# Kernel optimization log

Hardware: AMD Instinct MI355X
Metric: run time of the kernel (lower is better)

## Reference

```python
import jax, jax.numpy as jnp
import numpy as np

HIST, CNTX, PRED = 336, 168, 24
C = 1            # c_in == c_out == 1 (univariate)
HID = 128        # GRU hidden size
NFEAT = 5        # hourly time features (freq_map['H'])
EMB = 10 * NFEAT # embedding_dim * freq_map['H'] = 50
NLAGS = HIST - CNTX            # 168 lag taps
IN_DIM = EMB + NLAGS           # rnn input size = 218
NSAMP = 8192     # num_parallel_samples


def setup_inputs() -> dict:
    key = jax.random.key(0)
    ks = jax.random.split(key, 8)
    s = lambda fan: 1.0 / np.sqrt(fan)
    return {
        "x": jax.random.normal(ks[0], (1, HIST, C), jnp.float32),
        "x_mark": jax.random.normal(ks[1], (1, HIST, NFEAT), jnp.float32),
        "y_mark": jax.random.normal(ks[2], (1, PRED, NFEAT), jnp.float32),
        "W_emb": jax.random.normal(ks[3], (NFEAT, EMB), jnp.float32) * s(NFEAT),
        "b_emb": jnp.zeros((EMB,), jnp.float32),
        "W_ih": jax.random.normal(ks[4], (3 * HID, IN_DIM), jnp.float32) * s(IN_DIM),
        "W_hh": jax.random.normal(ks[5], (3 * HID, HID), jnp.float32) * s(HID),
        "b_ih": jnp.zeros((3 * HID,), jnp.float32),
        "b_hh": jnp.zeros((3 * HID,), jnp.float32),
        "W_proj": jax.random.normal(ks[6], (HID, 3), jnp.float32) * s(HID),
        "b_proj": jnp.zeros((3,), jnp.float32),
        "mode": 0,
    }


def reference(x, x_mark, y_mark, W_emb, b_emb, W_ih, W_hh, b_ih, b_hh, W_proj, b_proj, mode):

    def gru_step(h, xt):  # PyTorch GRU cell semantics (gate order r,z,n)
        gi = xt @ W_ih.T + b_ih
        gh = h @ W_hh.T + b_hh
        i_r, i_z, i_n = jnp.split(gi, 3, axis=-1)
        h_r, h_z, h_n = jnp.split(gh, 3, axis=-1)
        r = jax.nn.sigmoid(i_r + h_r)
        z = jax.nn.sigmoid(i_z + h_z)
        n = jnp.tanh(i_n + r * h_n)
        return (1.0 - z) * n + z * h

    B = x.shape[0]  # 1
    # ----- unroll_encoder (y=None path) -----
    # mean_abs_scaling over last cntx_len steps
    scale = jnp.clip(jnp.mean(jnp.abs(x[:, -CNTX:, :]), axis=1, keepdims=True), 1e-5, None)  # (B,1,C)
    xs = x / scale  # scaled sequence (lags/scale == lags of scaled sequence)
    # lagged subsequences: lag indices 1..NLAGS, subsequence length CNTX
    t_idx = (HIST - CNTX) + jnp.arange(CNTX)[:, None] - jnp.arange(1, NLAGS + 1)[None, :]  # (CNTX, NLAGS)
    lags = xs[:, t_idx, 0]  # (B, CNTX, NLAGS)  (C==1 so flatten is trivial)
    tf = x_mark[:, HIST - CNTX:, :] @ W_emb + b_emb  # (B, CNTX, EMB)
    enc_in = jnp.concatenate([lags, tf], axis=-1)  # (B, CNTX, IN_DIM)
    h0 = jnp.zeros((B, HID), x.dtype)
    h_last, _ = jax.lax.scan(lambda h, xt: (gru_step(h, xt), None), h0,
                             jnp.swapaxes(enc_in, 0, 1))  # final GRU state (B,HID)

    # ----- sampling_decoder -----
    sc = scale[0, 0, 0]  # scalar (B=1, C=1)
    h = jnp.broadcast_to(h_last, (NSAMP, HID))                       # repeat state over samples
    ym = jnp.broadcast_to(y_mark @ W_emb + b_emb, (NSAMP, PRED, EMB))  # repeated embedded marks
    buf = jnp.broadcast_to(x[0, -NLAGS:, 0], (NSAMP, NLAGS))         # last NLAGS observed values
    key0 = jax.random.key(42)

    def step(carry, ym_k):
        buf, h, key = carry
        key, sk = jax.random.split(key)
        lag_in = buf[:, ::-1] / sc                 # decoder lags: most recent first
        xin = jnp.concatenate([lag_in, ym_k], axis=-1)  # (S, IN_DIM)
        h = gru_step(h, xin)
        p = h @ W_proj + b_proj                    # (S, 3) StudentT arg projection
        df = 2.0 + jax.nn.softplus(p[:, 0])
        loc = p[:, 1]
        sigma = jax.nn.softplus(p[:, 2])
        t = jax.random.t(sk, df, shape=df.shape)
        samp = (loc + sigma * t) * sc              # affine-transformed StudentT sample
        buf = jnp.concatenate([buf[:, 1:], samp[:, None]], axis=1)
        return (buf, h, key), samp

    _, samples = jax.lax.scan(step, (buf, h, key0), jnp.swapaxes(ym, 0, 1))  # (PRED, S)
    return samples.T[:, :, None]  # (num_parallel_samples, pred_len, c_out)
```

## Files before the change

kernel.cpp:

```cpp
#include <hip/hip_runtime.h>
#include <stdint.h>

#define HIST 336
#define CNTX 168
#define PRED 24
#define HID 128
#define NFEAT 5
#define EMB 50
#define NLAGS 168
#define IN_DIM 218
#define NSAMP 8192
#define G3 384

#define WS_XS     0
#define WS_SC     336
#define WS_TF     340
#define WS_YM     8740
#define WS_KEYS   9940
#define WS_ENCGI  10036
#define WS_WQ     10036
#define WS_GISH   74548
#define WS_HLAST  83764
#define WS_WIHT   83892

__device__ __forceinline__ uint32_t rotl32(uint32_t v, int r){ return (v<<r)|(v>>(32-r)); }

__device__ __forceinline__ void threefry(uint32_t k0, uint32_t k1, uint32_t x0, uint32_t x1,
                                         uint32_t &o0, uint32_t &o1){
  uint32_t ks2 = k0 ^ k1 ^ 0x1BD11BDAu;
  x0 += k0; x1 += k1;
#define TFR(a) { x0 += x1; x1 = rotl32(x1,(a)); x1 ^= x0; }
  TFR(13) TFR(15) TFR(26) TFR(6)
  x0 += k1; x1 += ks2 + 1u;
  TFR(17) TFR(29) TFR(16) TFR(24)
  x0 += ks2; x1 += k0 + 2u;
  TFR(13) TFR(15) TFR(26) TFR(6)
  x0 += k0; x1 += k1 + 3u;
  TFR(17) TFR(29) TFR(16) TFR(24)
  x0 += k1; x1 += ks2 + 4u;
  TFR(13) TFR(15) TFR(26) TFR(6)
  x0 += ks2; x1 += k0 + 5u;
#undef TFR
  o0 = x0; o1 = x1;
}

__device__ __forceinline__ void tf_split2(uint32_t k0, uint32_t k1,
                                          uint32_t &a0, uint32_t &a1,
                                          uint32_t &b0, uint32_t &b1){
  threefry(k0,k1, 0u,0u, a0,a1);
  threefry(k0,k1, 0u,1u, b0,b1);
}

__device__ __forceinline__ void tf_split3(uint32_t k0, uint32_t k1,
                                          uint32_t &a0, uint32_t &a1,
                                          uint32_t &b0, uint32_t &b1,
                                          uint32_t &c0, uint32_t &c1){
  threefry(k0,k1, 0u,0u, a0,a1);
  threefry(k0,k1, 0u,1u, b0,b1);
  threefry(k0,k1, 0u,2u, c0,c1);
}

__device__ __forceinline__ uint32_t tf_bits1(uint32_t k0, uint32_t k1){
  uint32_t o0,o1; threefry(k0,k1, 0u,0u, o0,o1); return o0 ^ o1;
}

__device__ __forceinline__ uint32_t tf_bits_at(uint32_t k0, uint32_t k1, uint32_t i){
  uint32_t o0,o1; threefry(k0,k1, 0u,i, o0,o1); return o0 ^ o1;
}

__device__ __forceinline__ float bits_to_f01(uint32_t b){
  return __uint_as_float((b>>9) | 0x3f800000u) - 1.0f;
}

__device__ __forceinline__ float erfinv32(float x){
  float w = -log1pf(-x*x);
  float p;
  if (w < 5.0f){
    w = w - 2.5f;
    p = 2.81022636e-08f;
    p = fmaf(p, w, 3.43273939e-07f);
    p = fmaf(p, w, -3.5233877e-06f);
    p = fmaf(p, w, -4.39150654e-06f);
    p = fmaf(p, w, 0.00021858087f);
    p = fmaf(p, w, -0.00125372503f);
    p = fmaf(p, w, -0.00417768164f);
    p = fmaf(p, w, 0.246640727f);
    p = fmaf(p, w, 1.50140941f);
  } else {
    w = sqrtf(w) - 3.0f;
    p = -0.000200214257f;
    p = fmaf(p, w, 0.000100950558f);
    p = fmaf(p, w, 0.00134934322f);
    p = fmaf(p, w, -0.00367342844f);
    p = fmaf(p, w, 0.00573950773f);
    p = fmaf(p, w, -0.0076224613f);
    p = fmaf(p, w, 0.00943887047f);
    p = fmaf(p, w, 1.00167406f);
    p = fmaf(p, w, 2.83297682f);
  }
  return p*x;
}

__device__ __forceinline__ float normal_from_key(uint32_t k0, uint32_t k1){
  uint32_t b = tf_bits1(k0,k1);
  const float lo = -0.99999994f;
  float f = bits_to_f01(b);
  float u = fmaxf(lo, f*2.0f + lo);
  return 1.41421356f * erfinv32(u);
}

__device__ float gamma_sample(uint32_t k0, uint32_t k1, float alpha){
  float d = __fsub_rn(alpha, 0.33333334f);
  float c = 0.33333334f / sqrtf(d);
  uint32_t ck0,ck1, sb0,sb1;
  tf_split2(k0,k1, ck0,ck1, sb0,sb1);
  float V;
  for(;;){
    uint32_t nk0,nk1, xk0,xk1, uk0,uk1;
    tf_split3(ck0,ck1, nk0,nk1, xk0,xk1, uk0,uk1);
    ck0=nk0; ck1=nk1;
    float x, v;
    do {
      uint32_t xa0,xa1, xb0,xb1;
      tf_split2(xk0,xk1, xa0,xa1, xb0,xb1);
      xk0=xa0; xk1=xa1;
      x = normal_from_key(xb0,xb1);
      v = __fadd_rn(1.0f, __fmul_rn(x, c));
    } while (v <= 0.0f);
    float X  = __fmul_rn(x, x);
    float Vv = __fmul_rn(__fmul_rn(v, v), v);
    float U  = bits_to_f01(tf_bits1(uk0,uk1));
    float t1 = __fsub_rn(1.0f, __fmul_rn(0.0331f, __fmul_rn(X, X)));
    bool cont = (U >= t1);
    if (cont){
      float lhs = logf(U);
      float rhs = __fadd_rn(__fmul_rn(0.5f, X),
                  __fmul_rn(d, __fadd_rn(__fsub_rn(1.0f, Vv), logf(Vv))));
      cont = (lhs >= rhs);
    }
    if (!cont){ V = Vv; break; }
  }
  return d*V;
}

__device__ __forceinline__ float softplus_f(float x){
  float amax = fmaxf(x, 0.0f);
  return amax + log1pf(expf(-fabsf(x)));
}

__global__ __launch_bounds__(256) void k1_prep(const float* __restrict__ x,
                                               const float* __restrict__ xmark,
                                               const float* __restrict__ ymark,
                                               const float* __restrict__ Wemb,
                                               const float* __restrict__ bemb,
                                               float* __restrict__ ws){
  __shared__ float red[256];
  __shared__ float s_sc;
  int t = threadIdx.x;
  float a = 0.f;
  if (t < CNTX) a = fabsf(x[CNTX + t]);
  red[t] = a;
  __syncthreads();
  for(int s=128; s>0; s>>=1){ if(t<s) red[t]+=red[t+s]; __syncthreads(); }
  if (t==0){ s_sc = fmaxf(red[0]/168.0f, 1e-5f); ws[WS_SC]=s_sc; }
  __syncthreads();
  float sc = s_sc;
  for(int i=t; i<HIST; i+=256) ws[WS_XS+i] = x[i]/sc;
  for(int idx=t; idx<CNTX*EMB; idx+=256){
    int tt = idx/EMB, e = idx%EMB;
    float acc = bemb[e];
    for(int f=0; f<NFEAT; f++) acc += xmark[(CNTX+tt)*NFEAT+f]*Wemb[f*EMB+e];
    ws[WS_TF+idx] = acc;
  }
  for(int idx=t; idx<PRED*EMB; idx+=256){
    int kk = idx/EMB, e = idx%EMB;
    float acc = bemb[e];
    for(int f=0; f<NFEAT; f++) acc += ymark[kk*NFEAT+f]*Wemb[f*EMB+e];
    ws[WS_YM+idx] = acc;
  }
  if (t==0){
    uint32_t* kp = reinterpret_cast<uint32_t*>(ws + WS_KEYS);
    uint32_t c0 = 0u, c1 = 42u;
    for(int k=0;k<PRED;k++){
      uint32_t a0,a1,b0,b1;
      tf_split2(c0,c1, a0,a1, b0,b1);
      c0=a0; c1=a1;
      uint32_t n0,n1,g0,g1;
      tf_split2(b0,b1, n0,n1, g0,g1);
      kp[k*4+0]=n0; kp[k*4+1]=n1; kp[k*4+2]=g0; kp[k*4+3]=g1;
    }
  }
}

__global__ __launch_bounds__(256) void k2_gi(const float* __restrict__ Wih,
                                             const float* __restrict__ bih,
                                             const float* __restrict__ bhh,
                                             float* __restrict__ ws){
  int idx = blockIdx.x*256 + threadIdx.x;
  if (idx >= 192*G3) return;
  int t = idx / G3, r = idx % G3;
  const float* wr = Wih + r*IN_DIM;
  const float* xs = ws + WS_XS;
  float acc = bih[r] + (r < 256 ? bhh[r] : 0.0f);
  if (t < CNTX){
    const float* tf = ws + WS_TF + t*EMB;
    for(int j=0;j<NLAGS;j++) acc += wr[j]*xs[CNTX + t - 1 - j];
    for(int e=0;e<EMB;e++)   acc += wr[NLAGS+e]*tf[e];
    ws[WS_ENCGI + t*G3 + r] = acc;
  } else {
    int k = t - CNTX;
    const float* ym = ws + WS_YM + k*EMB;
    for(int e=0;e<EMB;e++)   acc += wr[NLAGS+e]*ym[e];
    for(int i=k;i<NLAGS;i++) acc += wr[i]*xs[HIST-1-i+k];
    ws[WS_GISH + k*G3 + r] = acc;
  }
}

__global__ __launch_bounds__(256) void k2b_wiht(const float* __restrict__ Wih,
                                                float* __restrict__ ws){
  int idx = blockIdx.x*256 + threadIdx.x;
  if (idx >= PRED*G3) return;
  int r = idx / PRED, i = idx % PRED;
  ws[WS_WIHT + i*G3 + r] = Wih[r*IN_DIM + i];
}

__global__ __launch_bounds__(384) void k3_enc(const float* __restrict__ Whh,
                                              const float* __restrict__ bhh,
                                              float* __restrict__ ws){
  __shared__ __align__(16) float h[HID];
  __shared__ float grz[256];
  __shared__ float hnv[HID];
  int r = threadIdx.x;
  float4 w[32];
  const float4* wr = (const float4*)(Whh + r*HID);
  #pragma unroll
  for(int i=0;i<32;i++) w[i] = wr[i];
  float bh = (r>=256)? bhh[r] : 0.0f;
  if (r < HID) h[r] = 0.0f;
  __syncthreads();
  const float* encgi = ws + WS_ENCGI;
  for(int t=0;t<CNTX;t++){
    float acc = 0.f;
    #pragma unroll
    for(int i=0;i<32;i++){
      float4 hv = *(const float4*)&h[4*i];
      float4 ww = w[i];
      acc = fmaf(ww.x,hv.x, fmaf(ww.y,hv.y, fmaf(ww.z,hv.z, fmaf(ww.w,hv.w, acc))));
    }
    if (r < 256) grz[r] = encgi[t*G3+r] + acc;
    else         hnv[r-256] = acc + bh;
    __syncthreads();
    if (r < HID){
      float rr = 1.0f/(1.0f+expf(-grz[r]));
      float zz = 1.0f/(1.0f+expf(-grz[128+r]));
      float inv = encgi[t*G3+256+r];
      float nn = tanhf(inv + rr*hnv[r]);
      h[r] = (1.0f-zz)*nn + zz*h[r];
    }
    __syncthreads();
  }
  if (r < HID) ws[WS_HLAST + r] = h[r];
}

__global__ __launch_bounds__(256) void k5_wq(const float* __restrict__ Whh,
                                             float* __restrict__ ws){
  int idx = blockIdx.x*256 + threadIdx.x;
  if (idx >= 32*G3) return;
  int q = idx / G3, r = idx % G3;
  float4 v = *(const float4*)&Whh[r*HID + q*4];
  ((float4*)(ws + WS_WQ))[idx] = v;
}

#define SPB 32
#define THR4 512
#define HROW 132

__global__ __launch_bounds__(512) void k4_dec(const float* __restrict__ Whh,
                                              const float* __restrict__ bhh,
                                              const float* __restrict__ Wproj,
                                              const float* __restrict__ bproj,
                                              const float* __restrict__ ws,
                                              float* __restrict__ out){
  __shared__ float g[G3][33];
  __shared__ float h[SPB][HROW];
  __shared__ float wihT_l[24*G3];
  __shared__ float shist[SPB][25];
  __shared__ float parr[SPB][4];
  __shared__ float wp[HID*3];
  __shared__ float bp[3];
  __shared__ uint32_t skeys[PRED*4];

  int t = threadIdx.x;
  int b = blockIdx.x;
  int rg = t & 127;
  int sg = t >> 7;
  int s0 = sg*8;

  float bhn = bhh[256 + rg];

  for(int idx=t; idx<24*G3; idx+=THR4) wihT_l[idx] = ws[WS_WIHT + idx];
  for(int idx=t; idx<HID*3; idx+=THR4) wp[idx] = Wproj[idx];
  if (t < 3) bp[t] = bproj[t];
  if (t < PRED*4) skeys[t] = reinterpret_cast<const uint32_t*>(ws + WS_KEYS)[t];
  if (t < HID){
    float hl = ws[WS_HLAST + t];
    for(int s=0;s<SPB;s++) h[s][t] = hl;
  }
  float sc = ws[WS_SC];
  const float* gish = ws + WS_GISH;
  const float4* Wq4 = (const float4*)(ws + WS_WQ);
  __syncthreads();

  #pragma unroll 1
  for(int k=0;k<PRED;k++){
    float aR_[8], aZ_[8], aH_[8];
    {
      float gR = gish[k*G3 + rg];
      float gZ = gish[k*G3 + 128 + rg];
      #pragma unroll
      for(int s=0;s<8;s++){ aR_[s]=gR; aZ_[s]=gZ; aH_[s]=bhn; }
    }
    #pragma unroll 1
    for(int i=0;i<k;i++){
      float wR = wihT_l[i*G3 + rg];
      float wZ = wihT_l[i*G3 + 128 + rg];
      #pragma unroll
      for(int s=0;s<8;s++){
        float sh = shist[s0+s][k-1-i];
        aR_[s] = fmaf(wR, sh, aR_[s]);
        aZ_[s] = fmaf(wZ, sh, aZ_[s]);
      }
    }
    #pragma unroll 1
    for(int q=0;q<32;q++){
      float4 wr4 = Wq4[q*G3 + rg];
      float4 wz4 = Wq4[q*G3 + 128 + rg];
      float4 wn4 = Wq4[q*G3 + 256 + rg];
      #pragma unroll
      for(int s=0;s<8;s++){
        float4 hv = *(const float4*)&h[s0+s][q*4];
        aR_[s] = fmaf(wr4.x, hv.x, aR_[s]); aR_[s] = fmaf(wr4.y, hv.y, aR_[s]);
        aR_[s] = fmaf(wr4.z, hv.z, aR_[s]); aR_[s] = fmaf(wr4.w, hv.w, aR_[s]);
        aZ_[s] = fmaf(wz4.x, hv.x, aZ_[s]); aZ_[s] = fmaf(wz4.y, hv.y, aZ_[s]);
        aZ_[s] = fmaf(wz4.z, hv.z, aZ_[s]); aZ_[s] = fmaf(wz4.w, hv.w, aZ_[s]);
        aH_[s] = fmaf(wn4.x, hv.x, aH_[s]); aH_[s] = fmaf(wn4.y, hv.y, aH_[s]);
        aH_[s] = fmaf(wn4.z, hv.z, aH_[s]); aH_[s] = fmaf(wn4.w, hv.w, aH_[s]);
      }
    }
    #pragma unroll
    for(int s=0;s<8;s++){
      g[rg][s0+s]       = aR_[s];
      g[128+rg][s0+s]   = aZ_[s];
      g[256+rg][s0+s]   = aH_[s];
    }
    __syncthreads();
    #pragma unroll 1
    for(int p=0;p<8;p++){
      int idx = t + p*THR4;
      int s = idx >> 7, j = idx & 127;
      float aRv = g[j][s], aZv = g[128+j][s], aHNv = g[256+j][s];
      float aINv = gish[k*G3 + 256 + j];
      #pragma unroll 1
      for(int i=0;i<k;i++)
        aINv = fmaf(wihT_l[i*G3 + 256 + j], shist[s][k-1-i], aINv);
      float rr = 1.0f/(1.0f+expf(-aRv));
      float zz = 1.0f/(1.0f+expf(-aZv));
      float nn = tanhf(aINv + rr*aHNv);
      h[s][j] = (1.0f-zz)*nn + zz*h[s][j];
    }
    __syncthreads();
    if (t < SPB*3){
      int s = t/3, c2 = t%3;
      float acc = bp[c2];
      for(int l=0;l<HID;l++) acc = fmaf(h[s][l], wp[l*3+c2], acc);
      parr[s][c2] = acc;
    }
    __syncthreads();
    if (t < SPB){
      int s = t, gs = b*SPB + s;
      float p0 = parr[s][0], loc = parr[s][1], p2 = parr[s][2];
      float df = 2.0f + softplus_f(p0);
      float half_df = df*0.5f;
      float sigma = softplus_f(p2);
      uint32_t kn0 = skeys[k*4+0], kn1 = skeys[k*4+1];
      uint32_t kg0 = skeys[k*4+2], kg1 = skeys[k*4+3];
      uint32_t bnb = tf_bits_at(kn0, kn1, (uint32_t)gs);
      const float lo = -0.99999994f;
      float un = fmaxf(lo, bits_to_f01(bnb)*2.0f + lo);
      float nval = 1.41421356f * erfinv32(un);
      uint32_t gk0, gk1;
      threefry(kg0, kg1, 0u, (uint32_t)gs, gk0, gk1);
      float gmm = gamma_sample(gk0, gk1, half_df);
      float tval = nval * sqrtf(half_df / gmm);
      float samp = (loc + sigma*tval)*sc;
      out[gs*PRED + k] = samp;
      shist[s][k] = samp / sc;
    }
    __syncthreads();
  }
}

extern "C" void kernel_launch(void* const* d_in, const int* in_sizes, int n_in,
                              void* d_out, int out_size, void* d_ws, size_t ws_size,
                              hipStream_t stream){
  const float* x     = (const float*)d_in[0];
  const float* xmark = (const float*)d_in[1];
  const float* ymark = (const float*)d_in[2];
  const float* Wemb  = (const float*)d_in[3];
  const float* bemb  = (const float*)d_in[4];
  const float* Wih   = (const float*)d_in[5];
  const float* Whh   = (const float*)d_in[6];
  const float* bih   = (const float*)d_in[7];
  const float* bhh   = (const float*)d_in[8];
  const float* Wproj = (const float*)d_in[9];
  const float* bproj = (const float*)d_in[10];
  float* ws  = (float*)d_ws;
  float* out = (float*)d_out;

  hipLaunchKernelGGL(k1_prep, dim3(1), dim3(256), 0, stream, x, xmark, ymark, Wemb, bemb, ws);
  hipLaunchKernelGGL(k2_gi, dim3(288), dim3(256), 0, stream, Wih, bih, bhh, ws);
  hipLaunchKernelGGL(k2b_wiht, dim3((PRED*G3+255)/256), dim3(256), 0, stream, Wih, ws);
  hipLaunchKernelGGL(k3_enc, dim3(1), dim3(384), 0, stream, Whh, bhh, ws);
  hipLaunchKernelGGL(k5_wq, dim3((32*G3+255)/256), dim3(256), 0, stream, Whh, ws);
  hipLaunchKernelGGL(k4_dec, dim3(NSAMP/SPB), dim3(THR4), 0, stream, Whh, bhh, Wproj, bproj, ws, out);
}
```

Before: 885.2 us.

## Keep GRU gate math in registers with transposed hidden state and packed FMA

The decoder kernel drops the shared gate buffer g. Each thread now applies the GRU nonlinearities to its own register accumulators and keeps its previous hidden values in registers (hold). The hidden state is stored transposed (hT4[row][sample-group]) so the matvec reads sample-contiguous float4s, and the accumulation uses 2-wide vector FMAs, which may lower to packed FP32 instructions. The input-lag contribution for the n gate moves into the same per-thread loop, removing a separate serial pass over the history. This cuts shared-memory traffic and one phase of work, at the cost of more live registers and a different LDS bank-access pattern.

```diff
diff --git a/kernel.cpp b/kernel.cpp
--- a/kernel.cpp
+++ b/kernel.cpp
@@ -22,6 +22,9 @@
 #define WS_GISH   74548
 #define WS_HLAST  83764
 #define WS_WIHT   83892
+
+typedef float v2f __attribute__((ext_vector_type(2)));
+__device__ __forceinline__ v2f fma2(v2f a, v2f b, v2f c){ return __builtin_elementwise_fma(a,b,c); }
 
 __device__ __forceinline__ uint32_t rotl32(uint32_t v, int r){ return (v<<r)|(v>>(32-r)); }
 
@@ -273,7 +276,6 @@
 
 #define SPB 32
 #define THR4 512
-#define HROW 132
 
 __global__ __launch_bounds__(512) void k4_dec(const float* __restrict__ Whh,
                                               const float* __restrict__ bhh,
@@ -281,10 +283,9 @@
                                               const float* __restrict__ bproj,
                                               const float* __restrict__ ws,
                                               float* __restrict__ out){
-  __shared__ float g[G3][33];
-  __shared__ float h[SPB][HROW];
+  __shared__ __align__(16) float4 hT4[128][9];
   __shared__ float wihT_l[24*G3];
-  __shared__ float shist[SPB][25];
+  __shared__ float shistT[25][34];
   __shared__ float parr[SPB][4];
   __shared__ float wp[HID*3];
   __shared__ float bp[3];
@@ -295,6 +296,7 @@
   int rg = t & 127;
   int sg = t >> 7;
   int s0 = sg*8;
+  int g0 = sg*2;
 
   float bhn = bhh[256 + rg];
 
@@ -302,9 +304,17 @@
   for(int idx=t; idx<HID*3; idx+=THR4) wp[idx] = Wproj[idx];
   if (t < 3) bp[t] = bproj[t];
   if (t < PRED*4) skeys[t] = reinterpret_cast<const uint32_t*>(ws + WS_KEYS)[t];
-  if (t < HID){
+  if (t < 128){
     float hl = ws[WS_HLAST + t];
-    for(int s=0;s<SPB;s++) h[s][t] = hl;
+    float4 v = {hl,hl,hl,hl};
+    #pragma unroll
+    for(int g=0;g<8;g++) hT4[t][g] = v;
+  }
+  float hold[8];
+  {
+    float hl = ws[WS_HLAST + rg];
+    #pragma unroll
+    for(int s=0;s<8;s++) hold[s] = hl;
   }
   float sc = ws[WS_SC];
   const float* gish = ws + WS_GISH;
@@ -313,22 +323,29 @@
 
   #pragma unroll 1
   for(int k=0;k<PRED;k++){
-    float aR_[8], aZ_[8], aH_[8];
+    v2f aR[4], aZ[4], aH[4], aI[4];
     {
       float gR = gish[k*G3 + rg];
       float gZ = gish[k*G3 + 128 + rg];
+      float gI = gish[k*G3 + 256 + rg];
       #pragma unroll
-      for(int s=0;s<8;s++){ aR_[s]=gR; aZ_[s]=gZ; aH_[s]=bhn; }
+      for(int p=0;p<4;p++){
+        aR[p] = (v2f){gR,gR}; aZ[p] = (v2f){gZ,gZ};
+        aI[p] = (v2f){gI,gI}; aH[p] = (v2f){bhn,bhn};
+      }
     }
     #pragma unroll 1
     for(int i=0;i<k;i++){
       float wR = wihT_l[i*G3 + rg];
       float wZ = wihT_l[i*G3 + 128 + rg];
+      float wN = wihT_l[i*G3 + 256 + rg];
+      v2f wR2 = {wR,wR}, wZ2 = {wZ,wZ}, wN2 = {wN,wN};
       #pragma unroll
-      for(int s=0;s<8;s++){
-        float sh = shist[s0+s][k-1-i];
-        aR_[s] = fmaf(wR, sh, aR_[s]);
-        aZ_[s] = fmaf(wZ, sh, aZ_[s]);
+      for(int p=0;p<4;p++){
+        v2f sh = *(const v2f*)&shistT[k-1-i][s0 + 2*p];
+        aR[p] = fma2(wR2, sh, aR[p]);
+        aZ[p] = fma2(wZ2, sh, aZ[p]);
+        aI[p] = fma2(wN2, sh, aI[p]);
       }
     }
     #pragma unroll 1
@@ -337,42 +354,42 @@
       float4 wz4 = Wq4[q*G3 + 128 + rg];
       float4 wn4 = Wq4[q*G3 + 256 + rg];
       #pragma unroll
-      for(int s=0;s<8;s++){
-        float4 hv = *(const float4*)&h[s0+s][q*4];
-        aR_[s] = fmaf(wr4.x, hv.x, aR_[s]); aR_[s] = fmaf(wr4.y, hv.y, aR_[s]);
-        aR_[s] = fmaf(wr4.z, hv.z, aR_[s]); aR_[s] = fmaf(wr4.w, hv.w, aR_[s]);
-        aZ_[s] = fmaf(wz4.x, hv.x, aZ_[s]); aZ_[s] = fmaf(wz4.y, hv.y, aZ_[s]);
-        aZ_[s] = fmaf(wz4.z, hv.z, aZ_[s]); aZ_[s] = fmaf(wz4.w, hv.w, aZ_[s]);
-        aH_[s] = fmaf(wn4.x, hv.x, aH_[s]); aH_[s] = fmaf(wn4.y, hv.y, aH_[s]);
-        aH_[s] = fmaf(wn4.z, hv.z, aH_[s]); aH_[s] = fmaf(wn4.w, hv.w, aH_[s]);
+      for(int c=0;c<4;c++){
+        float wrc = (c==0)?wr4.x:(c==1)?wr4.y:(c==2)?wr4.z:wr4.w;
+        float wzc = (c==0)?wz4.x:(c==1)?wz4.y:(c==2)?wz4.z:wz4.w;
+        float wnc = (c==0)?wn4.x:(c==1)?wn4.y:(c==2)?wn4.z:wn4.w;
+        v2f wr2 = {wrc,wrc}, wz2 = {wzc,wzc}, wn2 = {wnc,wnc};
+        #pragma unroll
+        for(int g=0;g<2;g++){
+          float4 hv = hT4[4*q + c][g0 + g];
+          v2f lo = {hv.x, hv.y}, hi = {hv.z, hv.w};
+          aR[2*g]   = fma2(wr2, lo, aR[2*g]);
+          aR[2*g+1] = fma2(wr2, hi, aR[2*g+1]);
+          aZ[2*g]   = fma2(wz2, lo, aZ[2*g]);
+          aZ[2*g+1] = fma2(wz2, hi, aZ[2*g+1]);
+          aH[2*g]   = fma2(wn2, lo, aH[2*g]);
+          aH[2*g+1] = fma2(wn2, hi, aH[2*g+1]);
+        }
       }
     }
+    __syncthreads();
     #pragma unroll
     for(int s=0;s<8;s++){
-      g[rg][s0+s]       = aR_[s];
-      g[128+rg][s0+s]   = aZ_[s];
-      g[256+rg][s0+s]   = aH_[s];
-    }
-    __syncthreads();
-    #pragma unroll 1
-    for(int p=0;p<8;p++){
-      int idx = t + p*THR4;
-      int s = idx >> 7, j = idx & 127;
-      float aRv = g[j][s], aZv = g[128+j][s], aHNv = g[256+j][s];
-      float aINv = gish[k*G3 + 256 + j];
-      #pragma unroll 1
-      for(int i=0;i<k;i++)
-        aINv = fmaf(wihT_l[i*G3 + 256 + j], shist[s][k-1-i], aINv);
+      int p = s >> 1, e = s & 1;
+      float aRv = aR[p][e], aZv = aZ[p][e], aIv = aI[p][e], aHv = aH[p][e];
       float rr = 1.0f/(1.0f+expf(-aRv));
       float zz = 1.0f/(1.0f+expf(-aZv));
-      float nn = tanhf(aINv + rr*aHNv);
-      h[s][j] = (1.0f-zz)*nn + zz*h[s][j];
+      float nn = tanhf(aIv + rr*aHv);
+      float hn = (1.0f-zz)*nn + zz*hold[s];
+      hold[s] = hn;
+      ((float*)&hT4[rg][g0 + (s>>2)])[s & 3] = hn;
     }
     __syncthreads();
     if (t < SPB*3){
       int s = t/3, c2 = t%3;
+      const float* hT = (const float*)hT4;
       float acc = bp[c2];
-      for(int l=0;l<HID;l++) acc = fmaf(h[s][l], wp[l*3+c2], acc);
+      for(int l=0;l<HID;l++) acc = fmaf(hT[l*36 + s], wp[l*3+c2], acc);
       parr[s][c2] = acc;
     }
     __syncthreads();
@@ -394,7 +411,7 @@
       float tval = nval * sqrtf(half_df / gmm);
       float samp = (loc + sigma*tval)*sc;
       out[gs*PRED + k] = samp;
-      shist[s][k] = samp / sc;
+      shistT[k][s] = samp / sc;
     }
     __syncthreads();
   }
```

Result: faster. 718.8 us, median of 2 (-18.8%).
